# Performance work log

Hardware: AMD Instinct MI355X
Metric: run time of the kernel (lower is better)

## Reference

```python
import jax, jax.numpy as jnp
import numpy as np

B, S, IN_F, OUT_F = 4, 2048, 4096, 4096
ALPHA = 0.01

def setup_inputs() -> dict:
    key = jax.random.key(0)
    k1, k2 = jax.random.split(key, 2)
    # int8-valued activations and weights (stored as int32 per harness dtype)
    x = jax.random.randint(k1, (B, S, IN_F), -127, 127, dtype=jnp.int32)
    weight = jax.random.randint(k2, (IN_F, OUT_F), -127, 127, dtype=jnp.int32)
    bias = jnp.zeros((1, OUT_F), dtype=jnp.float16)
    alpha = jnp.full((1,), ALPHA, dtype=jnp.float32)
    return {"x": x, "weight": weight, "bias": bias, "alpha": alpha}

def reference(x, weight, bias, alpha):
    # Faithful to forward's default (non-hybrid) path:
    # y = F.linear(x.float(), weight.t().float(), bias.float()) * alpha
    # F.linear(x, W^T) == x @ W, with W shape (in_features, out_features).
    x_shape = x.shape
    xf = x.reshape(-1, x_shape[-1]).astype(jnp.float32)          # [B*S, in]
    wf = weight.astype(jnp.float32)                               # [in, out]
    y = (xf @ wf + bias.astype(jnp.float32)) * alpha              # [B*S, out]
    return y.reshape(*x_shape[:-1], -1)                           # [B, S, out]
```

## Files before the change

### kernel.cpp

```cpp
#include <hip/hip_runtime.h>
#include <hip/hip_fp16.h>

using i32x4  = __attribute__((ext_vector_type(4)))  int;
using i32x16 = __attribute__((ext_vector_type(16))) int;

static constexpr int M  = 4 * 2048;
static constexpr int N  = 4096;
static constexpr int K  = 4096;
static constexpr int BM = 256, BN = 128, BK = 64;
static constexpr int NT = K / BK;
static constexpr int ATILE = BM * BK;
static constexpr int BTILE = BN * BK;

static constexpr int PX_BLOCKS = (int)((size_t)M * K / 16 / 256);
static constexpr int PW_BLOCKS = (int)((size_t)N * K / 16 / 256);

__device__ __forceinline__ unsigned pack4(i32x4 v) {
  return (unsigned)((v.x & 255) | ((v.y & 255) << 8) | ((v.z & 255) << 16) | (v.w << 24));
}

__global__ __launch_bounds__(256) void pack_kernel(const int* __restrict__ x,
                                                   const int* __restrict__ w,
                                                   unsigned char* __restrict__ wa,
                                                   unsigned char* __restrict__ wb) {
  if (blockIdx.x < PX_BLOCKS) {
    unsigned g = blockIdx.x * 256 + threadIdx.x;
    unsigned row = g & 255;
    unsigned kg  = (g >> 8) & 3;
    unsigned kt  = (g >> 10) & 63;
    unsigned br  = g >> 16;
    const int* src = x + ((size_t)(br * 256 + row) * K + kt * 64 + kg * 16);
    i32x4 v0 = *(const i32x4*)(src + 0);
    i32x4 v1 = *(const i32x4*)(src + 4);
    i32x4 v2 = *(const i32x4*)(src + 8);
    i32x4 v3 = *(const i32x4*)(src + 12);
    i32x4 d;
    d.x = (int)pack4(v0); d.y = (int)pack4(v1); d.z = (int)pack4(v2); d.w = (int)pack4(v3);
    *(i32x4*)(wa + (size_t)g * 16) = d;
  } else {
    unsigned g = (blockIdx.x - PX_BLOCKS) * 256 + threadIdx.x;
    unsigned col = g & 127;
    unsigned kg  = (g >> 7) & 3;
    unsigned kt  = (g >> 9) & 63;
    unsigned bn  = g >> 15;
    unsigned n   = bn * 128 + col;
    unsigned k0  = kt * 64 + kg * 16;
    const int* src = w + (size_t)k0 * N + n;
    i32x4 d;
#pragma unroll
    for (int j = 0; j < 4; ++j) {
      int b0 = src[(size_t)(j * 4 + 0) * N];
      int b1 = src[(size_t)(j * 4 + 1) * N];
      int b2 = src[(size_t)(j * 4 + 2) * N];
      int b3 = src[(size_t)(j * 4 + 3) * N];
      d[j] = (b0 & 255) | ((b1 & 255) << 8) | ((b2 & 255) << 16) | (b3 << 24);
    }
    *(i32x4*)(wb + (size_t)g * 16) = d;
  }
}


__global__ __launch_bounds__(256, 3) void gemm_i8(const unsigned char* __restrict__ wa,
                                                  const unsigned char* __restrict__ wb,
                                                  const __half* __restrict__ bias,
                                                  const float* __restrict__ alphaP,
                                                  float* __restrict__ out) {
  __shared__ __align__(16) unsigned char As[2][ATILE];
  __shared__ __align__(16) unsigned char Bs[2][BTILE];

  const int tid  = threadIdx.x;
  const int lane = tid & 63;
  const int w    = tid >> 6;
  const int wr   = w >> 1, wc = w & 1;
  const int l31  = lane & 31;
  const int kgl  = lane >> 5;

  const int bc = blockIdx.x;
  const int br = blockIdx.y;

  const unsigned char* ga = wa + (size_t)br * NT * ATILE;
  const unsigned char* gb = wb + (size_t)bc * NT * BTILE;

  i32x4 s0, s1, s2, s3, s4, s5;

#define GLOAD(T) do {                                                \
    const i32x4* ap = (const i32x4*)(ga + (size_t)(T) * ATILE);      \
    const i32x4* bp = (const i32x4*)(gb + (size_t)(T) * BTILE);      \
    s0 = ap[tid]; s1 = ap[tid + 256];                                \
    s2 = ap[tid + 512]; s3 = ap[tid + 768];                          \
    s4 = bp[tid]; s5 = bp[tid + 256];                                \
  } while (0)

#define SWRITE(BUF) do {                                             \
    i32x4* aw = (i32x4*)&As[BUF][0];                                 \
    i32x4* bw = (i32x4*)&Bs[BUF][0];                                 \
    aw[tid] = s0; aw[tid + 256] = s1;                                \
    aw[tid + 512] = s2; aw[tid + 768] = s3;                          \
    bw[tid] = s4; bw[tid + 256] = s5;                                \
  } while (0)

  GLOAD(0);
  SWRITE(0);
  __syncthreads();

  i32x16 acc[4][2] = {};

  const int arow = wr * 128 + l31;
  const int bcol = wc * 64 + l31;

  for (int t = 0; t < NT; ++t) {
    const int cur = t & 1;
    if (t + 1 < NT) GLOAD(t + 1);

    const unsigned char* Ab = &As[cur][0] + kgl * 4096;
    const unsigned char* Bb = &Bs[cur][0] + kgl * 2048;
#pragma unroll
    for (int kc = 0; kc < 2; ++kc) {
      const unsigned char* Ap = Ab + kc * 8192;
      const unsigned char* Bp = Bb + kc * 4096;
      i32x4 a0 = *(const i32x4*)(Ap + (arow +  0) * 16);
      i32x4 a1 = *(const i32x4*)(Ap + (arow + 32) * 16);
      i32x4 a2 = *(const i32x4*)(Ap + (arow + 64) * 16);
      i32x4 a3 = *(const i32x4*)(Ap + (arow + 96) * 16);
      i32x4 b0 = *(const i32x4*)(Bp + (bcol +  0) * 16);
      i32x4 b1 = *(const i32x4*)(Bp + (bcol + 32) * 16);
      acc[0][0] = __builtin_amdgcn_mfma_i32_32x32x32_i8(a0, b0, acc[0][0], 0, 0, 0);
      acc[0][1] = __builtin_amdgcn_mfma_i32_32x32x32_i8(a0, b1, acc[0][1], 0, 0, 0);
      acc[1][0] = __builtin_amdgcn_mfma_i32_32x32x32_i8(a1, b0, acc[1][0], 0, 0, 0);
      acc[1][1] = __builtin_amdgcn_mfma_i32_32x32x32_i8(a1, b1, acc[1][1], 0, 0, 0);
      acc[2][0] = __builtin_amdgcn_mfma_i32_32x32x32_i8(a2, b0, acc[2][0], 0, 0, 0);
      acc[2][1] = __builtin_amdgcn_mfma_i32_32x32x32_i8(a2, b1, acc[2][1], 0, 0, 0);
      acc[3][0] = __builtin_amdgcn_mfma_i32_32x32x32_i8(a3, b0, acc[3][0], 0, 0, 0);
      acc[3][1] = __builtin_amdgcn_mfma_i32_32x32x32_i8(a3, b1, acc[3][1], 0, 0, 0);
    }

    if (t + 1 < NT) SWRITE(cur ^ 1);
    __syncthreads();
  }

  const float alpha = *alphaP;
  const int row0 = br * 256 + wr * 128 + 4 * kgl;
  const int col0 = bc * 128 + wc * 64 + l31;
#pragma unroll
  for (int ni = 0; ni < 2; ++ni) {
    const int col = col0 + ni * 32;
    const float bf = __half2float(bias[col]);
#pragma unroll
    for (int mi = 0; mi < 4; ++mi) {
#pragma unroll
      for (int r = 0; r < 16; ++r) {
        const int row = row0 + mi * 32 + (r & 3) + 8 * (r >> 2);
        out[(size_t)row * N + col] = ((float)acc[mi][ni][r] + bf) * alpha;
      }
    }
  }
#undef GLOAD
#undef SWRITE
}

extern "C" void kernel_launch(void* const* d_in, const int* in_sizes, int n_in,
                              void* d_out, int out_size, void* d_ws, size_t ws_size,
                              hipStream_t stream) {
  const int*    x     = (const int*)d_in[0];
  const int*    wgt   = (const int*)d_in[1];
  const __half* bias  = (const __half*)d_in[2];
  const float*  alpha = (const float*)d_in[3];
  float*        out   = (float*)d_out;

  unsigned char* wa = (unsigned char*)d_ws;
  unsigned char* wb = wa + (size_t)M * K;

  pack_kernel<<<PX_BLOCKS + PW_BLOCKS, 256, 0, stream>>>(x, wgt, wa, wb);

  dim3 grid(N / BN, M / BM);
  gemm_i8<<<grid, 256, 0, stream>>>(wa, wb, bias, alpha, out);
}
```

Measured before the change: 246.2 us.

## Warp-specialize GEMM: producer waves stream A via direct-to-LDS loads, B from global

```diff
diff --git a/kernel.cpp b/kernel.cpp
--- a/kernel.cpp
+++ b/kernel.cpp
@@ -7,10 +7,10 @@
 static constexpr int M  = 4 * 2048;
 static constexpr int N  = 4096;
 static constexpr int K  = 4096;
-static constexpr int BM = 256, BN = 128, BK = 64;
-static constexpr int NT = K / BK;
-static constexpr int ATILE = BM * BK;
-static constexpr int BTILE = BN * BK;
+static constexpr int NT = K / 64;
+static constexpr int NDT = K / 128;
+static constexpr int ATILE = 256 * 64;
+static constexpr int BTILE = 128 * 64;
 
 static constexpr int PX_BLOCKS = (int)((size_t)M * K / 16 / 256);
 static constexpr int PW_BLOCKS = (int)((size_t)N * K / 16 / 256);
@@ -60,18 +60,27 @@
 }
 
 
-__global__ __launch_bounds__(256, 3) void gemm_i8(const unsigned char* __restrict__ wa,
+__device__ __forceinline__ void gload_lds16(const void* g, void* l) {
+  __builtin_amdgcn_global_load_lds((const __attribute__((address_space(1))) unsigned int*)g,
+                                   (__attribute__((address_space(3))) unsigned int*)l,
+                                   16, 0, 0);
+}
+
+#define FENCE()   asm volatile("" ::: "memory")
+#define BARRIER() do { FENCE(); __builtin_amdgcn_s_barrier(); FENCE(); } while (0)
+
+__global__ __launch_bounds__(512, 2) void gemm_i8(const unsigned char* __restrict__ wa,
                                                   const unsigned char* __restrict__ wb,
                                                   const __half* __restrict__ bias,
                                                   const float* __restrict__ alphaP,
                                                   float* __restrict__ out) {
-  __shared__ __align__(16) unsigned char As[2][ATILE];
-  __shared__ __align__(16) unsigned char Bs[2][BTILE];
+  __shared__ __align__(16) unsigned char As[3][32768];
 
   const int tid  = threadIdx.x;
   const int lane = tid & 63;
   const int w    = tid >> 6;
-  const int wr   = w >> 1, wc = w & 1;
+  const int cw   = w & 3;
+  const int cr   = cw >> 1, cc = cw & 1;
   const int l31  = lane & 31;
   const int kgl  = lane >> 5;
 
@@ -81,66 +90,91 @@
   const unsigned char* ga = wa + (size_t)br * NT * ATILE;
   const unsigned char* gb = wb + (size_t)bc * NT * BTILE;
 
-  i32x4 s0, s1, s2, s3, s4, s5;
-
-#define GLOAD(T) do {                                                \
-    const i32x4* ap = (const i32x4*)(ga + (size_t)(T) * ATILE);      \
-    const i32x4* bp = (const i32x4*)(gb + (size_t)(T) * BTILE);      \
-    s0 = ap[tid]; s1 = ap[tid + 256];                                \
-    s2 = ap[tid + 512]; s3 = ap[tid + 768];                          \
-    s4 = bp[tid]; s5 = bp[tid + 256];                                \
-  } while (0)
-
-#define SWRITE(BUF) do {                                             \
-    i32x4* aw = (i32x4*)&As[BUF][0];                                 \
-    i32x4* bw = (i32x4*)&Bs[BUF][0];                                 \
-    aw[tid] = s0; aw[tid + 256] = s1;                                \
-    aw[tid + 512] = s2; aw[tid + 768] = s3;                          \
-    bw[tid] = s4; bw[tid + 256] = s5;                                \
-  } while (0)
-
-  GLOAD(0);
-  SWRITE(0);
-  __syncthreads();
-
+  if (w >= 4) {
+    const int poff = cw * 8192;
+
+#define STAGE(DTI) do {                                                        \
+      const unsigned char* src = ga + (size_t)(DTI) * 32768 + poff + lane * 16; \
+      unsigned char* dst = &As[(DTI) % 3][poff];                               \
+      gload_lds16(src +    0, dst +    0);                                     \
+      gload_lds16(src + 1024, dst + 1024);                                     \
+      gload_lds16(src + 2048, dst + 2048);                                     \
+      gload_lds16(src + 3072, dst + 3072);                                     \
+      gload_lds16(src + 4096, dst + 4096);                                     \
+      gload_lds16(src + 5120, dst + 5120);                                     \
+      gload_lds16(src + 6144, dst + 6144);                                     \
+      gload_lds16(src + 7168, dst + 7168);                                     \
+    } while (0)
+
+    STAGE(0);
+    STAGE(1);
+    asm volatile("s_waitcnt vmcnt(8)" ::: "memory");
+    BARRIER();
+    for (int dt = 0; dt < NDT; ++dt) {
+      if (dt + 2 < NDT) STAGE(dt + 2);
+      if (dt + 2 < NDT)      asm volatile("s_waitcnt vmcnt(8)" ::: "memory");
+      else if (dt + 1 < NDT) asm volatile("s_waitcnt vmcnt(0)" ::: "memory");
+      BARRIER();
+    }
+#undef STAGE
+    return;
+  }
+
+  const int arow = cr * 128 + l31;
+  const int bcol = cc * 64 + l31;
+
+  i32x4 b[2][2][2][2];
   i32x16 acc[4][2] = {};
 
-  const int arow = wr * 128 + l31;
-  const int bcol = wc * 64 + l31;
-
-  for (int t = 0; t < NT; ++t) {
-    const int cur = t & 1;
-    if (t + 1 < NT) GLOAD(t + 1);
-
-    const unsigned char* Ab = &As[cur][0] + kgl * 4096;
-    const unsigned char* Bb = &Bs[cur][0] + kgl * 2048;
-#pragma unroll
-    for (int kc = 0; kc < 2; ++kc) {
-      const unsigned char* Ap = Ab + kc * 8192;
-      const unsigned char* Bp = Bb + kc * 4096;
-      i32x4 a0 = *(const i32x4*)(Ap + (arow +  0) * 16);
-      i32x4 a1 = *(const i32x4*)(Ap + (arow + 32) * 16);
-      i32x4 a2 = *(const i32x4*)(Ap + (arow + 64) * 16);
-      i32x4 a3 = *(const i32x4*)(Ap + (arow + 96) * 16);
-      i32x4 b0 = *(const i32x4*)(Bp + (bcol +  0) * 16);
-      i32x4 b1 = *(const i32x4*)(Bp + (bcol + 32) * 16);
-      acc[0][0] = __builtin_amdgcn_mfma_i32_32x32x32_i8(a0, b0, acc[0][0], 0, 0, 0);
-      acc[0][1] = __builtin_amdgcn_mfma_i32_32x32x32_i8(a0, b1, acc[0][1], 0, 0, 0);
-      acc[1][0] = __builtin_amdgcn_mfma_i32_32x32x32_i8(a1, b0, acc[1][0], 0, 0, 0);
-      acc[1][1] = __builtin_amdgcn_mfma_i32_32x32x32_i8(a1, b1, acc[1][1], 0, 0, 0);
-      acc[2][0] = __builtin_amdgcn_mfma_i32_32x32x32_i8(a2, b0, acc[2][0], 0, 0, 0);
-      acc[2][1] = __builtin_amdgcn_mfma_i32_32x32x32_i8(a2, b1, acc[2][1], 0, 0, 0);
-      acc[3][0] = __builtin_amdgcn_mfma_i32_32x32x32_i8(a3, b0, acc[3][0], 0, 0, 0);
-      acc[3][1] = __builtin_amdgcn_mfma_i32_32x32x32_i8(a3, b1, acc[3][1], 0, 0, 0);
-    }
-
-    if (t + 1 < NT) SWRITE(cur ^ 1);
-    __syncthreads();
+#define BLOADSUB(PAR, SUB, BASE) do {                                          \
+    b[PAR][SUB][0][0] = *(const i32x4*)((BASE) + (kgl)     * 2048 + (bcol +  0) * 16); \
+    b[PAR][SUB][0][1] = *(const i32x4*)((BASE) + (kgl)     * 2048 + (bcol + 32) * 16); \
+    b[PAR][SUB][1][0] = *(const i32x4*)((BASE) + (2 + kgl) * 2048 + (bcol +  0) * 16); \
+    b[PAR][SUB][1][1] = *(const i32x4*)((BASE) + (2 + kgl) * 2048 + (bcol + 32) * 16); \
+  } while (0)
+
+#define BLOAD(PAR, DT) do {                                                    \
+    const unsigned char* bt = gb + (size_t)(DT) * 16384;                       \
+    BLOADSUB(PAR, 0, bt);                                                      \
+    BLOADSUB(PAR, 1, bt + 8192);                                               \
+  } while (0)
+
+#define CHUNK(SLOT, SUB, KC, PAR) do {                                         \
+    const unsigned char* Ap = (SLOT) + (SUB) * 16384 + ((KC) * 2 + kgl) * 4096; \
+    i32x4 a0 = *(const i32x4*)(Ap + (arow +  0) * 16);                         \
+    i32x4 a1 = *(const i32x4*)(Ap + (arow + 32) * 16);                         \
+    i32x4 a2 = *(const i32x4*)(Ap + (arow + 64) * 16);                         \
+    i32x4 a3 = *(const i32x4*)(Ap + (arow + 96) * 16);                         \
+    acc[0][0] = __builtin_amdgcn_mfma_i32_32x32x32_i8(a0, b[PAR][SUB][KC][0], acc[0][0], 0, 0, 0); \
+    acc[0][1] = __builtin_amdgcn_mfma_i32_32x32x32_i8(a0, b[PAR][SUB][KC][1], acc[0][1], 0, 0, 0); \
+    acc[1][0] = __builtin_amdgcn_mfma_i32_32x32x32_i8(a1, b[PAR][SUB][KC][0], acc[1][0], 0, 0, 0); \
+    acc[1][1] = __builtin_amdgcn_mfma_i32_32x32x32_i8(a1, b[PAR][SUB][KC][1], acc[1][1], 0, 0, 0); \
+    acc[2][0] = __builtin_amdgcn_mfma_i32_32x32x32_i8(a2, b[PAR][SUB][KC][0], acc[2][0], 0, 0, 0); \
+    acc[2][1] = __builtin_amdgcn_mfma_i32_32x32x32_i8(a2, b[PAR][SUB][KC][1], acc[2][1], 0, 0, 0); \
+    acc[3][0] = __builtin_amdgcn_mfma_i32_32x32x32_i8(a3, b[PAR][SUB][KC][0], acc[3][0], 0, 0, 0); \
+    acc[3][1] = __builtin_amdgcn_mfma_i32_32x32x32_i8(a3, b[PAR][SUB][KC][1], acc[3][1], 0, 0, 0); \
+  } while (0)
+
+#define CSTEP(DT, PAR) do {                                                    \
+    if ((DT) + 1 < NDT) BLOAD(PAR ^ 1, (DT) + 1);    \
+    const unsigned char* slot = &As[(DT) % 3][0];                              \
+    CHUNK(slot, 0, 0, PAR);                                                    \
+    CHUNK(slot, 0, 1, PAR);                                                    \
+    CHUNK(slot, 1, 0, PAR);                                                    \
+    CHUNK(slot, 1, 1, PAR);                                                    \
+    BARRIER();                                                                 \
+  } while (0)
+
+  BLOAD(0, 0);
+  BARRIER();
+  for (int dt = 0; dt < NDT; dt += 2) {
+    CSTEP(dt, 0);
+    CSTEP(dt + 1, 1);
   }
 
   const float alpha = *alphaP;
-  const int row0 = br * 256 + wr * 128 + 4 * kgl;
-  const int col0 = bc * 128 + wc * 64 + l31;
+  const int row0 = br * 256 + cr * 128 + 4 * kgl;
+  const int col0 = bc * 128 + cc * 64 + l31;
 #pragma unroll
   for (int ni = 0; ni < 2; ++ni) {
     const int col = col0 + ni * 32;
@@ -154,8 +188,10 @@
       }
     }
   }
-#undef GLOAD
-#undef SWRITE
+#undef CSTEP
+#undef CHUNK
+#undef BLOAD
+#undef BLOADSUB
 }
 
 extern "C" void kernel_launch(void* const* d_in, const int* in_sizes, int n_in,
@@ -172,6 +208,6 @@
 
   pack_kernel<<<PX_BLOCKS + PW_BLOCKS, 256, 0, stream>>>(x, wgt, wa, wb);
 
-  dim3 grid(N / BN, M / BM);
-  gemm_i8<<<grid, 256, 0, stream>>>(wa, wb, bias, alpha, out);
-}
+  dim3 grid(N / 128, M / 256);
+  gemm_i8<<<grid, 512, 0, stream>>>(wa, wb, bias, alpha, out);
+}
```

Result: faster. 227.3 us (-7.7%).
